# Optimization experiments

Measured on AMD Instinct MI355X. Metric: run time of the kernel, lower is better.

The kernel has to match this reference:

```python
import jax, jax.numpy as jnp
import numpy as np

NUM_CLASSES = 21
NEGPOS_RATIO = 3
B, P = 64, 24564


def setup_inputs() -> dict:
    key = jax.random.key(0)
    ks = jax.random.split(key, 10)
    return {
        "loc_data": jax.random.normal(ks[0], (B, P, 4), jnp.float32),
        "conf_data": jax.random.normal(ks[1], (B, P, NUM_CLASSES), jnp.float32),
        "has_lp_data": jax.random.normal(ks[2], (B, P, 2), jnp.float32),
        "size_lp_data": jax.random.normal(ks[3], (B, P, 2), jnp.float32),
        "offset_data": jax.random.normal(ks[4], (B, P, 2), jnp.float32),
        "loc_t": jax.random.normal(ks[5], (B, P, 4), jnp.float32),
        "conf_t": jax.random.randint(ks[6], (B, P), 0, NUM_CLASSES, jnp.int64),
        "has_lp_t": jax.random.randint(ks[7], (B, P), 0, 2, jnp.int64),
        "size_lp_t": jax.random.normal(ks[8], (B, P, 2), jnp.float32),
        "offset_t": jax.random.normal(ks[9], (B, P, 2), jnp.float32),
    }


def _smooth_l1_sum(p, t, mask):
    # sum-reduced smooth L1 (beta=1) over elements selected by mask
    d = jnp.abs(p - t)
    l = jnp.where(d < 1.0, 0.5 * d * d, d - 0.5)
    return jnp.sum(l * mask)


def _ce_per_row(logits, labels):
    # per-row cross entropy: logsumexp(logits) - logits[label]
    lse = jax.nn.logsumexp(logits, axis=-1)
    g = jnp.take_along_axis(logits, labels[..., None], axis=-1)[..., 0]
    return lse - g


def reference(loc_data, conf_data, has_lp_data, size_lp_data, offset_data,
              loc_t, conf_t, has_lp_t, size_lp_t, offset_t):
    dt = loc_data.dtype
    num_priors = conf_data.shape[1]
    pos = conf_t > 0                                  # [B,P]
    posf = pos.astype(dt)[..., None]                  # [B,P,1]

    # localization loss over positives
    loss_l = _smooth_l1_sum(loc_data, loc_t, posf)

    # size / offset losses over positives, gated by has_lp flag
    hlp = has_lp_t.astype(dt)[..., None]              # [B,P,1]
    loss_size_lp = _smooth_l1_sum(size_lp_data * hlp, size_lp_t * hlp, posf)
    loss_offset = _smooth_l1_sum(offset_data * hlp, offset_t * hlp, posf)

    # hard negative mining on per-prior conf CE
    ce = _ce_per_row(conf_data, conf_t)               # [B,P]
    ce_mine = jnp.where(pos, 0.0, ce)
    loss_idx = jnp.argsort(-ce_mine, axis=1)          # descending sort indices
    idx_rank = jnp.argsort(loss_idx, axis=1)          # rank of each prior
    num_pos = jnp.sum(pos, axis=1, keepdims=True)     # [B,1]
    num_neg = jnp.clip(NEGPOS_RATIO * num_pos, None, num_priors - 1)
    neg = idx_rank < num_neg                          # [B,P]
    sel = (pos | neg).astype(dt)

    loss_c = jnp.sum(ce * sel)
    loss_has_lp = jnp.sum(_ce_per_row(has_lp_data, has_lp_t) * sel)

    N = jnp.sum(pos).astype(dt)
    return (loss_l / N, loss_c / N, loss_size_lp / N,
            loss_offset / N, loss_has_lp / N)
```

## Files before the change

### kernel.cpp

```cpp
#include <hip/hip_runtime.h>
#include <stdint.h>

#define NC 21
#define BATCH 64
#define PRI 24564
#define NROWS (BATCH * PRI)
#define SLABS 32
#define SLABR 768
#define GBLK (BATCH * SLABS)
#define CHUNK 96

typedef float f4a4 __attribute__((ext_vector_type(4), aligned(4)));

__device__ __forceinline__ float sl1f(float p, float t) {
    float d = fabsf(p - t);
    return d < 1.0f ? 0.5f * d * d : d - 0.5f;
}

__device__ __forceinline__ unsigned int f2k(float v) {
    unsigned int u = __float_as_uint(v);
    return (u & 0x80000000u) ? ~u : (u | 0x80000000u);
}

__device__ __forceinline__ unsigned int chkey(float2 ch) {
    unsigned hb = __float_as_uint(ch.y);
    return (hb & 0x80000000u) ? 0x80000000u : f2k(ch.x);
}

__device__ __forceinline__ double blockReduce(double v, double* sred) {
    #pragma unroll
    for (int off = 32; off > 0; off >>= 1)
        v += __shfl_down(v, off, 64);
    const int wid = threadIdx.x >> 6, lane = threadIdx.x & 63;
    __syncthreads();
    if (lane == 0) sred[wid] = v;
    __syncthreads();
    double r = 0.0;
    if (threadIdx.x == 0) r = sred[0] + sred[1] + sred[2] + sred[3];
    return r;
}

__global__ __launch_bounds__(256, 4) void k_main(
    const float* __restrict__ loc_data, const float* __restrict__ conf_data,
    const float* __restrict__ has_lp_data, const float* __restrict__ size_lp_data,
    const float* __restrict__ offset_data, const float* __restrict__ loc_t,
    const int* __restrict__ conf_t, const int* __restrict__ has_lp_t,
    const float* __restrict__ size_lp_t, const float* __restrict__ offset_t,
    float2* __restrict__ ws_ch, int* __restrict__ numpos, double* __restrict__ part,
    int* __restrict__ ghist1)
{
    __shared__ int hist[4096];
    __shared__ double sred[4];
    const int tid = threadIdx.x;
    const int b = blockIdx.x >> 5, s = blockIdx.x & 31;
    for (int k = tid; k < 4096; k += 256) hist[k] = 0;
    __syncthreads();

    int pr[3]; bool vld[3];
    #pragma unroll
    for (int i = 0; i < 3; ++i) {
        int p = s * SLABR + i * 256 + tid;
        vld[i] = p < PRI;
        pr[i] = vld[i] ? p : PRI - 1;
    }
    const unsigned rb = (unsigned)b * PRI;

    int ct[3];
    #pragma unroll
    for (int i = 0; i < 3; ++i) ct[i] = conf_t[rb + pr[i]];
    f4a4 cw[3][5]; float c20[3], gg[3];
    #pragma unroll
    for (int i = 0; i < 3; ++i) {
        const float* crow = conf_data + (long)(rb + pr[i]) * NC;
        #pragma unroll
        for (int j = 0; j < 5; ++j) cw[i][j] = ((const f4a4*)crow)[j];
        c20[i] = crow[20];
        gg[i] = crow[ct[i]];
    }
    float ce[3];
    #pragma unroll
    for (int i = 0; i < 3; ++i) {
        float m = c20[i];
        #pragma unroll
        for (int j = 0; j < 5; ++j)
            m = fmaxf(m, fmaxf(fmaxf(cw[i][j].x, cw[i][j].y), fmaxf(cw[i][j].z, cw[i][j].w)));
        float sum = __expf(c20[i] - m);
        #pragma unroll
        for (int j = 0; j < 5; ++j)
            sum += __expf(cw[i][j].x - m) + __expf(cw[i][j].y - m)
                 + __expf(cw[i][j].z - m) + __expf(cw[i][j].w - m);
        ce[i] = m + __logf(sum) - gg[i];
    }
    #pragma unroll
    for (int i = 0; i < 3; ++i) {
        if (vld[i] && ct[i] <= 0) {
            unsigned key = f2k(ce[i]);
            if (key != 0x80000000u) atomicAdd(&hist[key >> 20], 1);
        }
    }

    int hl[3]; float4 lp[3], lt[3]; float2 sp2[3], st2[3], op2[3], ot2[3], hh[3];
    #pragma unroll
    for (int i = 0; i < 3; ++i) {
        const unsigned r = rb + pr[i];
        hl[i] = has_lp_t[r];
        lp[i] = ((const float4*)loc_data)[r];
        lt[i] = ((const float4*)loc_t)[r];
        sp2[i] = ((const float2*)size_lp_data)[r];
        st2[i] = ((const float2*)size_lp_t)[r];
        op2[i] = ((const float2*)offset_data)[r];
        ot2[i] = ((const float2*)offset_t)[r];
        hh[i] = ((const float2*)has_lp_data)[r];
    }
    double aL = 0.0, aS = 0.0, aO = 0.0;
    int myp = 0;
    #pragma unroll
    for (int i = 0; i < 3; ++i) {
        const bool pos = ct[i] > 0;
        float ll = sl1f(lp[i].x, lt[i].x) + sl1f(lp[i].y, lt[i].y)
                 + sl1f(lp[i].z, lt[i].z) + sl1f(lp[i].w, lt[i].w);
        float ls = sl1f(sp2[i].x, st2[i].x) + sl1f(sp2[i].y, st2[i].y);
        float lo = sl1f(op2[i].x, ot2[i].x) + sl1f(op2[i].y, ot2[i].y);
        const float pf = (vld[i] && pos) ? 1.f : 0.f;
        const float hf = (hl[i] != 0) ? 1.f : 0.f;
        aL += (double)(pf * ll);
        aS += (double)(pf * hf * ls);
        aO += (double)(pf * hf * lo);
        float hm = fmaxf(hh[i].x, hh[i].y);
        float hs = __expf(hh[i].x - hm) + __expf(hh[i].y - hm);
        float hlce = fmaxf(hm + __logf(hs) - (hl[i] != 0 ? hh[i].y : hh[i].x), 0.0f);
        unsigned hb = __float_as_uint(hlce) | (pos ? 0x80000000u : 0u);
        if (vld[i]) ws_ch[rb + pr[i]] = make_float2(ce[i], __uint_as_float(hb));
        myp += (vld[i] && pos) ? 1 : 0;
    }

    double v;
    v = blockReduce(aL, sred); if (tid == 0) part[0 * GBLK + blockIdx.x] = v;
    v = blockReduce(aS, sred); if (tid == 0) part[1 * GBLK + blockIdx.x] = v;
    v = blockReduce(aO, sred); if (tid == 0) part[2 * GBLK + blockIdx.x] = v;
    v = blockReduce((double)myp, sred);
    if (tid == 0 && v > 0.0) atomicAdd(&numpos[b], (int)(v + 0.5));

    __syncthreads();
    for (int k = tid; k < 4096; k += 256) {
        int h = hist[k];
        if (h) atomicAdd(&ghist1[(b << 12) + k], h);
    }
}

__global__ __launch_bounds__(256) void k_batch(
    const float2* __restrict__ ws_ch, const int* __restrict__ ghist1,
    const int* __restrict__ numpos, double* __restrict__ lossCH)
{
    const int b = blockIdx.x, tid = threadIdx.x;
    __shared__ int sct[256];
    __shared__ int shist[1024];
    __shared__ double sred[4];
    __shared__ unsigned s_dig;
    __shared__ int s_rem;
    __shared__ int s_cut;

    const float2* row = ws_ch + (unsigned)b * PRI;

    int K = 3 * numpos[b]; if (K > PRI - 1) K = PRI - 1;
    int h[16];
    {
        const int* g = ghist1 + (b << 12) + tid * 16;
        int ctn = 0;
        #pragma unroll
        for (int j = 0; j < 16; ++j) { h[j] = g[j]; ctn += h[j]; }
        sct[tid] = ctn;
    }
    __syncthreads();
    #pragma unroll
    for (int off = 1; off < 256; off <<= 1) {
        int v = (tid + off < 256) ? sct[tid + off] : 0;
        __syncthreads();
        sct[tid] += v;
        __syncthreads();
    }
    const int M = sct[0];

    unsigned T; int need;
    if (K <= 0) {
        T = 0xFFFFFFFFu; need = 0;
    } else if (K > M) {
        T = 0x80000000u; need = K - M;
    } else {
        const int Safter = (tid < 255) ? sct[tid + 1] : 0;
        int cum = Safter;
        #pragma unroll
        for (int j = 15; j >= 0; --j) {
            int c2 = cum + h[j];
            if (c2 >= K && cum < K) { s_dig = (unsigned)(tid * 16 + j); s_rem = K - cum; }
            cum = c2;
        }
        __syncthreads();
        unsigned pref = s_dig; int rem = s_rem;

        for (int k = tid; k < 1024; k += 256) shist[k] = 0;
        __syncthreads();
        for (int p = tid; p < PRI; p += 256) {
            unsigned key = chkey(row[p]);
            if (key != 0x80000000u && (key >> 20) == pref)
                atomicAdd(&shist[(key >> 10) & 1023], 1);
        }
        __syncthreads();
        {
            int h4[4]; int c4 = 0;
            #pragma unroll
            for (int j = 0; j < 4; ++j) { h4[j] = shist[tid * 4 + j]; c4 += h4[j]; }
            __syncthreads();
            sct[tid] = c4;
            __syncthreads();
            #pragma unroll
            for (int off = 1; off < 256; off <<= 1) {
                int v = (tid + off < 256) ? sct[tid + off] : 0;
                __syncthreads();
                sct[tid] += v;
                __syncthreads();
            }
            const int Sa = (tid < 255) ? sct[tid + 1] : 0;
            int cum2 = Sa;
            #pragma unroll
            for (int j = 3; j >= 0; --j) {
                int c2 = cum2 + h4[j];
                if (c2 >= rem && cum2 < rem) { s_dig = (unsigned)(tid * 4 + j); s_rem = rem - cum2; }
                cum2 = c2;
            }
            __syncthreads();
        }
        pref = (pref << 10) | s_dig; rem = s_rem;
        __syncthreads();

        for (int k = tid; k < 1024; k += 256) shist[k] = 0;
        __syncthreads();
        for (int p = tid; p < PRI; p += 256) {
            unsigned key = chkey(row[p]);
            if (key != 0x80000000u && (key >> 10) == pref)
                atomicAdd(&shist[key & 1023], 1);
        }
        __syncthreads();
        {
            int h4[4]; int c4 = 0;
            #pragma unroll
            for (int j = 0; j < 4; ++j) { h4[j] = shist[tid * 4 + j]; c4 += h4[j]; }
            __syncthreads();
            sct[tid] = c4;
            __syncthreads();
            #pragma unroll
            for (int off = 1; off < 256; off <<= 1) {
                int v = (tid + off < 256) ? sct[tid + off] : 0;
                __syncthreads();
                sct[tid] += v;
                __syncthreads();
            }
            const int Sa = (tid < 255) ? sct[tid + 1] : 0;
            int cum2 = Sa;
            #pragma unroll
            for (int j = 3; j >= 0; --j) {
                int c2 = cum2 + h4[j];
                if (c2 >= rem && cum2 < rem) { s_dig = (unsigned)(tid * 4 + j); s_rem = rem - cum2; }
                cum2 = c2;
            }
            __syncthreads();
        }
        T = (pref << 10) | s_dig; need = s_rem;
        __syncthreads();
    }

    double aC = 0.0, aH = 0.0;
    for (int p = tid; p < PRI; p += 256) {
        float2 ch = row[p];
        unsigned hb = __float_as_uint(ch.y);
        const bool pos = (hb >> 31) != 0;
        const unsigned key = pos ? 0x80000000u : f2k(ch.x);
        const float hlv = __uint_as_float(hb & 0x7fffffffu);
        if (pos || key > T) { aC += (double)ch.x; aH += (double)hlv; }
    }

    if (tid == 0) s_cut = -1;
    __syncthreads();
    const int c0 = tid * CHUNK;
    const int c1 = (c0 + CHUNK < PRI) ? c0 + CHUNK : PRI;
    int tcnt = 0;
    if (need > 0) {
        for (int p = c0; p < c1; ++p) tcnt += (chkey(row[p]) == T) ? 1 : 0;
    }
    sct[tid] = tcnt;
    __syncthreads();
    #pragma unroll
    for (int off = 1; off < 256; off <<= 1) {
        int v = (tid >= off) ? sct[tid - off] : 0;
        __syncthreads();
        sct[tid] += v;
        __syncthreads();
    }
    if (need > 0) {
        const int incl = sct[tid], excl = incl - tcnt;
        if (excl < need && need <= incl) {
            int want = need - excl, c = 0;
            for (int p = c0; p < c1; ++p) {
                if (chkey(row[p]) == T) { ++c; if (c == want) { s_cut = p; break; } }
            }
        }
    }
    __syncthreads();
    const int cutoff = s_cut;

    double tCn = 0.0, tHn = 0.0;
    for (int p = tid; p <= cutoff; p += 256) {
        float2 ch = row[p];
        unsigned hb = __float_as_uint(ch.y);
        const bool pos = (hb >> 31) != 0;
        if (!pos) {
            const unsigned key = f2k(ch.x);
            if (key == T) {
                tCn += (double)ch.x;
                tHn += (double)__uint_as_float(hb & 0x7fffffffu);
            }
        }
    }

    double totC = blockReduce(aC + tCn, sred);
    double totH = blockReduce(aH + tHn, sred);
    if (tid == 0) { lossCH[b] = totC; lossCH[64 + b] = totH; }
}

__global__ __launch_bounds__(256) void k_final(
    const double* __restrict__ part, const int* __restrict__ numpos,
    const double* __restrict__ lossCH, float* __restrict__ out)
{
    __shared__ double sred[4];
    const int tid = threadIdx.x;
    double s[3];
    #pragma unroll
    for (int k = 0; k < 3; ++k) {
        double a = 0.0;
        for (int t = tid; t < GBLK; t += 256) a += part[k * GBLK + t];
        s[k] = blockReduce(a, sred);
    }
    double lc = (tid < BATCH) ? lossCH[tid] : 0.0;
    lc = blockReduce(lc, sred);
    double lh = (tid < BATCH) ? lossCH[64 + tid] : 0.0;
    lh = blockReduce(lh, sred);
    double n = (tid < BATCH) ? (double)numpos[tid] : 0.0;
    n = blockReduce(n, sred);
    if (tid == 0) {
        out[0] = (float)(s[0] / n);
        out[1] = (float)(lc / n);
        out[2] = (float)(s[1] / n);
        out[3] = (float)(s[2] / n);
        out[4] = (float)(lh / n);
    }
}

extern "C" void kernel_launch(void* const* d_in, const int* in_sizes, int n_in,
                              void* d_out, int out_size, void* d_ws, size_t ws_size,
                              hipStream_t stream)
{
    const float* loc_data     = (const float*)d_in[0];
    const float* conf_data    = (const float*)d_in[1];
    const float* has_lp_data  = (const float*)d_in[2];
    const float* size_lp_data = (const float*)d_in[3];
    const float* offset_data  = (const float*)d_in[4];
    const float* loc_t        = (const float*)d_in[5];
    const int*   conf_t       = (const int*)d_in[6];
    const int*   has_lp_t     = (const int*)d_in[7];
    const float* size_lp_t    = (const float*)d_in[8];
    const float* offset_t     = (const float*)d_in[9];
    float* out = (float*)d_out;

    char* ws = (char*)d_ws;
    int* numpos      = (int*)(ws + 0);
    double* part     = (double*)(ws + 16384);
    double* lossCH   = (double*)(ws + 131072);
    int* ghist1      = (int*)(ws + 132096);
    float2* ws_ch    = (float2*)(ws + 1704960);

    hipMemsetAsync(ws, 0, 256, stream);
    hipMemsetAsync(ws + 132096, 0, 1048576, stream);

    k_main<<<GBLK, 256, 0, stream>>>(loc_data, conf_data, has_lp_data, size_lp_data,
                                     offset_data, loc_t, conf_t, has_lp_t,
                                     size_lp_t, offset_t, ws_ch, numpos, part, ghist1);
    k_batch<<<BATCH, 256, 0, stream>>>(ws_ch, ghist1, numpos, lossCH);
    k_final<<<1, 256, 0, stream>>>(part, numpos, lossCH, out);
}
```

Measured before the change: 385.8 us.

## Move top-level histogram into per-batch select kernel and widen it to 1024 threads

The first-level radix histogram and the atomic num-positive counter leave the main kernel, which drops its 16KB shared histogram, global atomics and the two memsets, and now runs with a higher occupancy bound. The per-batch selection kernel grows to 1024 threads and builds the 12-bit histogram itself. It then refines with 10-bit digit passes and resolves ties at the threshold with a ballot-based stripe scan instead of a serial chunk scan. This trades one extra pass over the per-batch workspace for less atomic traffic and more parallelism in the 64-block select stage.

```diff
diff --git a/kernel.cpp b/kernel.cpp
--- a/kernel.cpp
+++ b/kernel.cpp
@@ -8,7 +8,9 @@
 #define SLABS 32
 #define SLABR 768
 #define GBLK (BATCH * SLABS)
-#define CHUNK 96
+#define BTHR 1024
+#define BITER 24
+#define NSTRIPE (BITER * 16)
 
 typedef float f4a4 __attribute__((ext_vector_type(4), aligned(4)));
 
@@ -22,11 +24,6 @@
     return (u & 0x80000000u) ? ~u : (u | 0x80000000u);
 }
 
-__device__ __forceinline__ unsigned int chkey(float2 ch) {
-    unsigned hb = __float_as_uint(ch.y);
-    return (hb & 0x80000000u) ? 0x80000000u : f2k(ch.x);
-}
-
 __device__ __forceinline__ double blockReduce(double v, double* sred) {
     #pragma unroll
     for (int off = 32; off > 0; off >>= 1)
@@ -40,21 +37,34 @@
     return r;
 }
 
-__global__ __launch_bounds__(256, 4) void k_main(
+__device__ __forceinline__ double bred16(double v, double* sred) {
+    #pragma unroll
+    for (int off = 32; off > 0; off >>= 1)
+        v += __shfl_down(v, off, 64);
+    const int wid = threadIdx.x >> 6, lane = threadIdx.x & 63;
+    __syncthreads();
+    if (lane == 0) sred[wid] = v;
+    __syncthreads();
+    double r = 0.0;
+    if (threadIdx.x == 0) {
+        #pragma unroll
+        for (int i = 0; i < 16; ++i) r += sred[i];
+    }
+    __syncthreads();
+    return r;
+}
+
+__global__ __launch_bounds__(256, 8) void k_main(
     const float* __restrict__ loc_data, const float* __restrict__ conf_data,
     const float* __restrict__ has_lp_data, const float* __restrict__ size_lp_data,
     const float* __restrict__ offset_data, const float* __restrict__ loc_t,
     const int* __restrict__ conf_t, const int* __restrict__ has_lp_t,
     const float* __restrict__ size_lp_t, const float* __restrict__ offset_t,
-    float2* __restrict__ ws_ch, int* __restrict__ numpos, double* __restrict__ part,
-    int* __restrict__ ghist1)
+    float2* __restrict__ ws_ch, double* __restrict__ part)
 {
-    __shared__ int hist[4096];
     __shared__ double sred[4];
     const int tid = threadIdx.x;
     const int b = blockIdx.x >> 5, s = blockIdx.x & 31;
-    for (int k = tid; k < 4096; k += 256) hist[k] = 0;
-    __syncthreads();
 
     int pr[3]; bool vld[3];
     #pragma unroll
@@ -90,13 +100,6 @@
             sum += __expf(cw[i][j].x - m) + __expf(cw[i][j].y - m)
                  + __expf(cw[i][j].z - m) + __expf(cw[i][j].w - m);
         ce[i] = m + __logf(sum) - gg[i];
-    }
-    #pragma unroll
-    for (int i = 0; i < 3; ++i) {
-        if (vld[i] && ct[i] <= 0) {
-            unsigned key = f2k(ce[i]);
-            if (key != 0x80000000u) atomicAdd(&hist[key >> 20], 1);
-        }
     }
 
     int hl[3]; float4 lp[3], lt[3]; float2 sp2[3], st2[3], op2[3], ot2[3], hh[3];
@@ -139,130 +142,165 @@
     v = blockReduce(aS, sred); if (tid == 0) part[1 * GBLK + blockIdx.x] = v;
     v = blockReduce(aO, sred); if (tid == 0) part[2 * GBLK + blockIdx.x] = v;
     v = blockReduce((double)myp, sred);
-    if (tid == 0 && v > 0.0) atomicAdd(&numpos[b], (int)(v + 0.5));
-
-    __syncthreads();
-    for (int k = tid; k < 4096; k += 256) {
-        int h = hist[k];
-        if (h) atomicAdd(&ghist1[(b << 12) + k], h);
-    }
-}
-
-__global__ __launch_bounds__(256) void k_batch(
-    const float2* __restrict__ ws_ch, const int* __restrict__ ghist1,
-    const int* __restrict__ numpos, double* __restrict__ lossCH)
+    if (tid == 0) part[3 * GBLK + blockIdx.x] = v;
+}
+
+__global__ __launch_bounds__(BTHR) void k_batch(
+    const float2* __restrict__ ws_ch, const double* __restrict__ part,
+    double* __restrict__ lossCH)
 {
     const int b = blockIdx.x, tid = threadIdx.x;
-    __shared__ int sct[256];
-    __shared__ int shist[1024];
-    __shared__ double sred[4];
+    const int lane = tid & 63, wid = tid >> 6;
+    __shared__ int shist[4096];
+    __shared__ int sct[BTHR];
+    __shared__ int sCnt[NSTRIPE];
+    __shared__ double sTC[NSTRIPE], sTH[NSTRIPE];
+    __shared__ double sred[16];
+    __shared__ double s_np;
+    __shared__ int s_M;
     __shared__ unsigned s_dig;
     __shared__ int s_rem;
-    __shared__ int s_cut;
+    __shared__ int s_st, s_loc;
 
     const float2* row = ws_ch + (unsigned)b * PRI;
 
-    int K = 3 * numpos[b]; if (K > PRI - 1) K = PRI - 1;
-    int h[16];
     {
-        const int* g = ghist1 + (b << 12) + tid * 16;
-        int ctn = 0;
-        #pragma unroll
-        for (int j = 0; j < 16; ++j) { h[j] = g[j]; ctn += h[j]; }
-        sct[tid] = ctn;
-    }
-    __syncthreads();
-    #pragma unroll
-    for (int off = 1; off < 256; off <<= 1) {
-        int v = (tid + off < 256) ? sct[tid + off] : 0;
-        __syncthreads();
-        sct[tid] += v;
-        __syncthreads();
-    }
-    const int M = sct[0];
+        double np = 0.0;
+        if (tid < 32) np = part[3 * GBLK + b * 32 + tid];
+        #pragma unroll
+        for (int off = 32; off > 0; off >>= 1) np += __shfl_down(np, off, 64);
+        if (tid == 0) s_np = np;
+    }
+    __syncthreads();
+    int K = 3 * (int)(s_np + 0.5);
+    if (K > PRI - 1) K = PRI - 1;
+
+    if (K <= 0) {
+        if (tid == 0) { lossCH[b] = 0.0; lossCH[64 + b] = 0.0; }
+        return;
+    }
+
+    {
+        int mc = 0;
+        for (int i = 0; i < BITER; ++i) {
+            const int p = i * BTHR + tid;
+            if (p < PRI) {
+                float2 ch = row[p];
+                unsigned hb = __float_as_uint(ch.y);
+                if (!(hb >> 31) && f2k(ch.x) != 0x80000000u) ++mc;
+            }
+        }
+        double Md = bred16((double)mc, sred);
+        if (tid == 0) s_M = (int)(Md + 0.5);
+    }
+    __syncthreads();
+    const int M = s_M;
 
     unsigned T; int need;
-    if (K <= 0) {
-        T = 0xFFFFFFFFu; need = 0;
-    } else if (K > M) {
+    if (K > M) {
         T = 0x80000000u; need = K - M;
     } else {
-        const int Safter = (tid < 255) ? sct[tid + 1] : 0;
-        int cum = Safter;
-        #pragma unroll
-        for (int j = 15; j >= 0; --j) {
-            int c2 = cum + h[j];
-            if (c2 >= K && cum < K) { s_dig = (unsigned)(tid * 16 + j); s_rem = K - cum; }
-            cum = c2;
-        }
-        __syncthreads();
-        unsigned pref = s_dig; int rem = s_rem;
-
-        for (int k = tid; k < 1024; k += 256) shist[k] = 0;
-        __syncthreads();
-        for (int p = tid; p < PRI; p += 256) {
-            unsigned key = chkey(row[p]);
-            if (key != 0x80000000u && (key >> 20) == pref)
-                atomicAdd(&shist[(key >> 10) & 1023], 1);
+        for (int k = tid; k < 4096; k += BTHR) shist[k] = 0;
+        __syncthreads();
+        for (int i = 0; i < BITER; ++i) {
+            const int p = i * BTHR + tid;
+            if (p < PRI) {
+                float2 ch = row[p];
+                unsigned hb = __float_as_uint(ch.y);
+                if (!(hb >> 31)) {
+                    unsigned key = f2k(ch.x);
+                    if (key != 0x80000000u) atomicAdd(&shist[key >> 20], 1);
+                }
+            }
         }
         __syncthreads();
         {
-            int h4[4]; int c4 = 0;
+            int h4[4]; int ctn = 0;
             #pragma unroll
-            for (int j = 0; j < 4; ++j) { h4[j] = shist[tid * 4 + j]; c4 += h4[j]; }
-            __syncthreads();
-            sct[tid] = c4;
+            for (int j = 0; j < 4; ++j) { h4[j] = shist[tid * 4 + j]; ctn += h4[j]; }
+            sct[tid] = ctn;
             __syncthreads();
             #pragma unroll
-            for (int off = 1; off < 256; off <<= 1) {
-                int v = (tid + off < 256) ? sct[tid + off] : 0;
+            for (int off = 1; off < BTHR; off <<= 1) {
+                int v = (tid + off < BTHR) ? sct[tid + off] : 0;
                 __syncthreads();
                 sct[tid] += v;
                 __syncthreads();
             }
-            const int Sa = (tid < 255) ? sct[tid + 1] : 0;
-            int cum2 = Sa;
+            const int Sa = (tid < BTHR - 1) ? sct[tid + 1] : 0;
+            int cum = Sa;
             #pragma unroll
             for (int j = 3; j >= 0; --j) {
-                int c2 = cum2 + h4[j];
-                if (c2 >= rem && cum2 < rem) { s_dig = (unsigned)(tid * 4 + j); s_rem = rem - cum2; }
-                cum2 = c2;
-            }
+                int c2 = cum + h4[j];
+                if (c2 >= K && cum < K) { s_dig = (unsigned)(tid * 4 + j); s_rem = K - cum; }
+                cum = c2;
+            }
+            __syncthreads();
+        }
+        unsigned pref = s_dig; int rem = s_rem;
+        __syncthreads();
+
+        if (tid < 1024) shist[tid] = 0;
+        __syncthreads();
+        for (int i = 0; i < BITER; ++i) {
+            const int p = i * BTHR + tid;
+            if (p < PRI) {
+                float2 ch = row[p];
+                unsigned hb = __float_as_uint(ch.y);
+                if (!(hb >> 31)) {
+                    unsigned key = f2k(ch.x);
+                    if (key != 0x80000000u && (key >> 20) == pref)
+                        atomicAdd(&shist[(key >> 10) & 1023], 1);
+                }
+            }
+        }
+        __syncthreads();
+        {
+            const int hb1 = shist[tid];
+            sct[tid] = hb1;
+            __syncthreads();
+            #pragma unroll
+            for (int off = 1; off < BTHR; off <<= 1) {
+                int v = (tid + off < BTHR) ? sct[tid + off] : 0;
+                __syncthreads();
+                sct[tid] += v;
+                __syncthreads();
+            }
+            const int Sa = (tid < BTHR - 1) ? sct[tid + 1] : 0;
+            if (Sa + hb1 >= rem && Sa < rem) { s_dig = (unsigned)tid; s_rem = rem - Sa; }
             __syncthreads();
         }
         pref = (pref << 10) | s_dig; rem = s_rem;
         __syncthreads();
 
-        for (int k = tid; k < 1024; k += 256) shist[k] = 0;
-        __syncthreads();
-        for (int p = tid; p < PRI; p += 256) {
-            unsigned key = chkey(row[p]);
-            if (key != 0x80000000u && (key >> 10) == pref)
-                atomicAdd(&shist[key & 1023], 1);
+        if (tid < 1024) shist[tid] = 0;
+        __syncthreads();
+        for (int i = 0; i < BITER; ++i) {
+            const int p = i * BTHR + tid;
+            if (p < PRI) {
+                float2 ch = row[p];
+                unsigned hb = __float_as_uint(ch.y);
+                if (!(hb >> 31)) {
+                    unsigned key = f2k(ch.x);
+                    if (key != 0x80000000u && (key >> 10) == pref)
+                        atomicAdd(&shist[key & 1023], 1);
+                }
+            }
         }
         __syncthreads();
         {
-            int h4[4]; int c4 = 0;
+            const int hb1 = shist[tid];
+            sct[tid] = hb1;
+            __syncthreads();
             #pragma unroll
-            for (int j = 0; j < 4; ++j) { h4[j] = shist[tid * 4 + j]; c4 += h4[j]; }
-            __syncthreads();
-            sct[tid] = c4;
-            __syncthreads();
-            #pragma unroll
-            for (int off = 1; off < 256; off <<= 1) {
-                int v = (tid + off < 256) ? sct[tid + off] : 0;
+            for (int off = 1; off < BTHR; off <<= 1) {
+                int v = (tid + off < BTHR) ? sct[tid + off] : 0;
                 __syncthreads();
                 sct[tid] += v;
                 __syncthreads();
             }
-            const int Sa = (tid < 255) ? sct[tid + 1] : 0;
-            int cum2 = Sa;
-            #pragma unroll
-            for (int j = 3; j >= 0; --j) {
-                int c2 = cum2 + h4[j];
-                if (c2 >= rem && cum2 < rem) { s_dig = (unsigned)(tid * 4 + j); s_rem = rem - cum2; }
-                cum2 = c2;
-            }
+            const int Sa = (tid < BTHR - 1) ? sct[tid + 1] : 0;
+            if (Sa + hb1 >= rem && Sa < rem) { s_dig = (unsigned)tid; s_rem = rem - Sa; }
             __syncthreads();
         }
         T = (pref << 10) | s_dig; need = s_rem;
@@ -270,66 +308,86 @@
     }
 
     double aC = 0.0, aH = 0.0;
-    for (int p = tid; p < PRI; p += 256) {
-        float2 ch = row[p];
-        unsigned hb = __float_as_uint(ch.y);
+    for (int i = 0; i < BITER; ++i) {
+        const int p = i * BTHR + tid;
+        const bool valid = p < PRI;
+        float2 ch = valid ? row[p] : make_float2(0.f, 0.f);
+        const unsigned hb = __float_as_uint(ch.y);
         const bool pos = (hb >> 31) != 0;
         const unsigned key = pos ? 0x80000000u : f2k(ch.x);
         const float hlv = __uint_as_float(hb & 0x7fffffffu);
-        if (pos || key > T) { aC += (double)ch.x; aH += (double)hlv; }
-    }
-
-    if (tid == 0) s_cut = -1;
-    __syncthreads();
-    const int c0 = tid * CHUNK;
-    const int c1 = (c0 + CHUNK < PRI) ? c0 + CHUNK : PRI;
-    int tcnt = 0;
-    if (need > 0) {
-        for (int p = c0; p < c1; ++p) tcnt += (chkey(row[p]) == T) ? 1 : 0;
-    }
-    sct[tid] = tcnt;
-    __syncthreads();
-    #pragma unroll
-    for (int off = 1; off < 256; off <<= 1) {
-        int v = (tid >= off) ? sct[tid - off] : 0;
-        __syncthreads();
-        sct[tid] += v;
-        __syncthreads();
-    }
-    if (need > 0) {
-        const int incl = sct[tid], excl = incl - tcnt;
-        if (excl < need && need <= incl) {
-            int want = need - excl, c = 0;
-            for (int p = c0; p < c1; ++p) {
-                if (chkey(row[p]) == T) { ++c; if (c == want) { s_cut = p; break; } }
-            }
-        }
-    }
-    __syncthreads();
-    const int cutoff = s_cut;
-
-    double tCn = 0.0, tHn = 0.0;
-    for (int p = tid; p <= cutoff; p += 256) {
-        float2 ch = row[p];
-        unsigned hb = __float_as_uint(ch.y);
+        if (valid && (pos || key > T)) { aC += (double)ch.x; aH += (double)hlv; }
+        const bool eq = valid && (key == T);
+        const unsigned long long msk = __ballot(eq);
+        double tc = (eq && !pos) ? (double)ch.x : 0.0;
+        double th = (eq && !pos) ? (double)hlv : 0.0;
+        #pragma unroll
+        for (int off = 32; off > 0; off >>= 1) {
+            tc += __shfl_down(tc, off, 64);
+            th += __shfl_down(th, off, 64);
+        }
+        if (lane == 0) {
+            sCnt[i * 16 + wid] = (int)__popcll(msk);
+            sTC[i * 16 + wid] = tc;
+            sTH[i * 16 + wid] = th;
+        }
+    }
+    const double aCt = bred16(aC, sred);
+    const double aHt = bred16(aH, sred);
+
+    double accC = 0.0, accH = 0.0;
+    if (tid == 0) {
+        int st = -1, loc = 0, cum = 0;
+        if (need > 0) {
+            for (int s2 = 0; s2 < NSTRIPE; ++s2) {
+                const int c = sCnt[s2];
+                if (cum + c >= need) { st = s2; loc = need - cum; break; }
+                cum += c;
+                accC += sTC[s2]; accH += sTH[s2];
+            }
+        }
+        s_st = st; s_loc = loc;
+    }
+    __syncthreads();
+    const int st = s_st, loc = s_loc;
+
+    double pC = 0.0, pH = 0.0;
+    if (wid == 0 && st >= 0) {
+        const int base = (st >> 4) * BTHR + (st & 15) * 64;
+        const int p = base + lane;
+        const bool valid = p < PRI;
+        float2 ch = valid ? row[p] : make_float2(0.f, 0.f);
+        const unsigned hb = __float_as_uint(ch.y);
         const bool pos = (hb >> 31) != 0;
-        if (!pos) {
-            const unsigned key = f2k(ch.x);
-            if (key == T) {
-                tCn += (double)ch.x;
-                tHn += (double)__uint_as_float(hb & 0x7fffffffu);
-            }
-        }
-    }
-
-    double totC = blockReduce(aC + tCn, sred);
-    double totH = blockReduce(aH + tHn, sred);
-    if (tid == 0) { lossCH[b] = totC; lossCH[64 + b] = totH; }
+        const unsigned key = pos ? 0x80000000u : f2k(ch.x);
+        const float hlv = __uint_as_float(hb & 0x7fffffffu);
+        const bool eq = valid && (key == T);
+        const unsigned long long msk = __ballot(eq);
+        const int rank = (int)__popcll(msk & ((1ull << lane) - 1ull)) + 1;
+        int sel = (eq && rank == loc) ? lane : 64;
+        #pragma unroll
+        for (int off = 32; off > 0; off >>= 1) {
+            int o = __shfl_xor(sel, off, 64);
+            sel = (o < sel) ? o : sel;
+        }
+        const bool take = eq && !pos && (lane <= sel);
+        pC = take ? (double)ch.x : 0.0;
+        pH = take ? (double)hlv : 0.0;
+        #pragma unroll
+        for (int off = 32; off > 0; off >>= 1) {
+            pC += __shfl_down(pC, off, 64);
+            pH += __shfl_down(pH, off, 64);
+        }
+    }
+    if (tid == 0) {
+        lossCH[b] = aCt + accC + pC;
+        lossCH[64 + b] = aHt + accH + pH;
+    }
 }
 
 __global__ __launch_bounds__(256) void k_final(
-    const double* __restrict__ part, const int* __restrict__ numpos,
-    const double* __restrict__ lossCH, float* __restrict__ out)
+    const double* __restrict__ part, const double* __restrict__ lossCH,
+    float* __restrict__ out)
 {
     __shared__ double sred[4];
     const int tid = threadIdx.x;
@@ -340,12 +398,13 @@
         for (int t = tid; t < GBLK; t += 256) a += part[k * GBLK + t];
         s[k] = blockReduce(a, sred);
     }
+    double a = 0.0;
+    for (int t = tid; t < GBLK; t += 256) a += part[3 * GBLK + t];
+    double n = blockReduce(a, sred);
     double lc = (tid < BATCH) ? lossCH[tid] : 0.0;
     lc = blockReduce(lc, sred);
     double lh = (tid < BATCH) ? lossCH[64 + tid] : 0.0;
     lh = blockReduce(lh, sred);
-    double n = (tid < BATCH) ? (double)numpos[tid] : 0.0;
-    n = blockReduce(n, sred);
     if (tid == 0) {
         out[0] = (float)(s[0] / n);
         out[1] = (float)(lc / n);
@@ -372,18 +431,13 @@
     float* out = (float*)d_out;
 
     char* ws = (char*)d_ws;
-    int* numpos      = (int*)(ws + 0);
     double* part     = (double*)(ws + 16384);
     double* lossCH   = (double*)(ws + 131072);
-    int* ghist1      = (int*)(ws + 132096);
     float2* ws_ch    = (float2*)(ws + 1704960);
-
-    hipMemsetAsync(ws, 0, 256, stream);
-    hipMemsetAsync(ws + 132096, 0, 1048576, stream);
 
     k_main<<<GBLK, 256, 0, stream>>>(loc_data, conf_data, has_lp_data, size_lp_data,
                                      offset_data, loc_t, conf_t, has_lp_t,
-                                     size_lp_t, offset_t, ws_ch, numpos, part, ghist1);
-    k_batch<<<BATCH, 256, 0, stream>>>(ws_ch, ghist1, numpos, lossCH);
-    k_final<<<1, 256, 0, stream>>>(part, numpos, lossCH, out);
-}
+                                     size_lp_t, offset_t, ws_ch, part);
+    k_batch<<<BATCH, BTHR, 0, stream>>>(ws_ch, part, lossCH);
+    k_final<<<1, 256, 0, stream>>>(part, lossCH, out);
+}
```

New measurement: 478.5 us. +24.0%, slower.
